# Optimization experiments

Measured on AMD Instinct MI355X. Metric: run time of the kernel, lower is better.

## Reference

```python
import jax, jax.numpy as jnp
import numpy as np

B, S, H = 2, 2048, 4096
NH, NKV, D = 32, 8, 128          # query heads, kv heads, head_dim = H // NH
G = NH // NKV                    # GQA group size
THETA = 10000.0


def setup_inputs() -> dict:
    key = jax.random.key(0)
    k1, k2, k3 = jax.random.split(key, 3)
    hidden_states = jax.random.normal(k1, (B, S, H), dtype=jnp.float32)
    positions = jnp.tile(jnp.arange(S, dtype=jnp.int64 if jax.config.jax_enable_x64 else jnp.int32), (B, 1))
    w_qkv = jax.random.normal(k2, (H, (NH + 2 * NKV) * D), dtype=jnp.float32) * 0.02
    w_o = jax.random.normal(k3, (NH * D, H), dtype=jnp.float32) * 0.02
    return {"hidden_states": hidden_states, "positions": positions, "w_qkv": w_qkv, "w_o": w_o}


def _rope_interleaved(x, positions, theta):
    # is_neox_style=False: rotate interleaved (even, odd) pairs. x: [B,S,Hh,D]
    d = x.shape[-1]
    inv_freq = 1.0 / (theta ** (jnp.arange(0, d, 2, dtype=jnp.float32) / d))  # [D/2]
    freqs = positions.astype(jnp.float32)[..., None] * inv_freq               # [B,S,D/2]
    cos = jnp.cos(freqs)[:, :, None, :]
    sin = jnp.sin(freqs)[:, :, None, :]
    x1 = x[..., 0::2]
    x2 = x[..., 1::2]
    o1 = x1 * cos - x2 * sin
    o2 = x2 * cos + x1 * sin
    return jnp.stack([o1, o2], axis=-1).reshape(x.shape)


def reference(hidden_states, positions, w_qkv, w_o):
    qkv = hidden_states @ w_qkv                                   # [B,S,(NH+2*NKV)*D]
    q, k, v = jnp.split(qkv, [NH * D, NH * D + NKV * D], axis=-1)
    q = q.reshape(B, S, NH, D)
    k = k.reshape(B, S, NKV, D)
    v = v.reshape(B, S, NKV, D)
    q = _rope_interleaved(q, positions, THETA)
    k = _rope_interleaved(k, positions, THETA)
    # GQA: group query heads per kv head instead of repeating k/v
    qg = q.reshape(B, S, NKV, G, D)
    scores = jnp.einsum('bqhgd,bkhd->bhgqk', qg, k) * (D ** -0.5)  # [B,NKV,G,S,S]
    causal = jnp.tril(jnp.ones((S, S), dtype=bool))
    scores = jnp.where(causal, scores, jnp.finfo(scores.dtype).min)
    probs = jax.nn.softmax(scores, axis=-1)
    out = jnp.einsum('bhgqk,bkhd->bqhgd', probs, v).reshape(B, S, NH * D)
    return out @ w_o                                              # [B,S,H]
```

## Files before the change

### kernel.cpp

```cpp
#include <hip/hip_runtime.h>
#include <cmath>

#define B_    2
#define S_    2048
#define H_    4096
#define NH_   32
#define NKV_  8
#define D_    128
#define QKV_N 6144
#define MTOK  4096

typedef __attribute__((ext_vector_type(8))) short bf16x8;
typedef __attribute__((ext_vector_type(4))) float f32x4;
typedef __attribute__((ext_vector_type(4))) unsigned short us4;

#define GLL16(gp, lp)                                                         \
  __builtin_amdgcn_global_load_lds(                                           \
      (const __attribute__((address_space(1))) void*)(gp),                    \
      (__attribute__((address_space(3))) void*)(lp), 16, 0, 0)

__device__ __forceinline__ unsigned short f2bf(float f) {
  unsigned u = __float_as_uint(f);
  u += 0x7fff + ((u >> 16) & 1);
  return (unsigned short)(u >> 16);
}

__global__ __launch_bounds__(256) void cast_bf16_kernel(const float* __restrict__ in,
                                                        unsigned short* __restrict__ out,
                                                        int n4) {
  int i = blockIdx.x * blockDim.x + threadIdx.x;
  if (i >= n4) return;
  float4 v = ((const float4*)in)[i];
  us4 o;
  o.x = f2bf(v.x); o.y = f2bf(v.y); o.z = f2bf(v.z); o.w = f2bf(v.w);
  ((us4*)out)[i] = o;
}

__global__ __launch_bounds__(256) void transpose_cast_kernel(const float* __restrict__ w,
                                                             unsigned short* __restrict__ wt,
                                                             int K, int N) {
  __shared__ float tile[32][33];
  const int k0 = blockIdx.y * 32, n0 = blockIdx.x * 32;
  const int tid = threadIdx.x;
  const int r = tid >> 3, c4 = (tid & 7) * 4;
  float4 v = *(const float4*)(w + (size_t)(k0 + r) * N + n0 + c4);
  tile[r][c4 + 0] = v.x; tile[r][c4 + 1] = v.y;
  tile[r][c4 + 2] = v.z; tile[r][c4 + 3] = v.w;
  __syncthreads();
  us4 o;
  o.x = f2bf(tile[c4 + 0][r]);
  o.y = f2bf(tile[c4 + 1][r]);
  o.z = f2bf(tile[c4 + 2][r]);
  o.w = f2bf(tile[c4 + 3][r]);
  *(us4*)(wt + (size_t)(n0 + r) * K + k0 + c4) = o;
}

__global__ __launch_bounds__(256) void gemm_bt_kernel(const unsigned short* __restrict__ A,
                                                      const unsigned short* __restrict__ Bt,
                                                      float* __restrict__ C,
                                                      int M, int N, int K) {
  __shared__ short As[128 * 32];
  __shared__ short Bs[128 * 32];
  const int tid = threadIdx.x;
  const int w = tid >> 6, lane = tid & 63;
  const int quad = lane >> 4, l16 = lane & 15;
  const int bm = blockIdx.y, bn = blockIdx.x;
  const int mbase = (w & 1) * 64, nbase = (w >> 1) * 64;

  f32x4 acc[4][4] = {};

  const int srow = w * 32 + (lane >> 2);
  const int skoff = (lane & 3) * 8;
  const unsigned short* Ap = A + (size_t)(bm * 128 + srow) * K + skoff;
  const unsigned short* Bp = Bt + (size_t)(bn * 128 + srow) * K + skoff;

  for (int k0 = 0; k0 < K; k0 += 32) {
    __syncthreads();
#pragma unroll
    for (int i = 0; i < 2; ++i) {
      GLL16(Ap + (size_t)i * 16 * K + k0, As + (w * 32 + i * 16) * 32);
      GLL16(Bp + (size_t)i * 16 * K + k0, Bs + (w * 32 + i * 16) * 32);
    }
    __syncthreads();
    bf16x8 af[4], bfr[4];
#pragma unroll
    for (int mi = 0; mi < 4; ++mi)
      af[mi] = *(const bf16x8*)(As + (mbase + mi * 16 + l16) * 32 + quad * 8);
#pragma unroll
    for (int nj = 0; nj < 4; ++nj)
      bfr[nj] = *(const bf16x8*)(Bs + (nbase + nj * 16 + l16) * 32 + quad * 8);
#pragma unroll
    for (int mi = 0; mi < 4; ++mi)
#pragma unroll
      for (int nj = 0; nj < 4; ++nj)
        acc[mi][nj] = __builtin_amdgcn_mfma_f32_16x16x32_bf16(af[mi], bfr[nj], acc[mi][nj], 0, 0, 0);
  }

  float* Cp = C + (size_t)(bm * 128 + mbase + quad * 4) * N + bn * 128 + nbase + l16;
#pragma unroll
  for (int mi = 0; mi < 4; ++mi)
#pragma unroll
    for (int nj = 0; nj < 4; ++nj)
#pragma unroll
      for (int r = 0; r < 4; ++r)
        Cp[(size_t)(mi * 16 + r) * N + nj * 16] = acc[mi][nj][r];
}

__global__ __launch_bounds__(256) void rope_cast_kernel(const float* __restrict__ qkv,
                                                        const int* __restrict__ positions,
                                                        unsigned short* __restrict__ qkvb) {
  const int tok = blockIdx.y;
  const int p = blockIdx.x * 256 + threadIdx.x;
  const float2 x = *(const float2*)(qkv + (size_t)tok * QKV_N + 2 * p);
  float o1, o2;
  if (p < (NH_ + NKV_) * (D_ / 2)) {
    const int j = p & 63;
    const float inv = exp2f((float)(2 * j) * (-13.287712379549449f / 128.f));
    const float f = (float)positions[tok] * inv;
    float s, c;
    sincosf(f, &s, &c);
    o1 = x.x * c - x.y * s;
    o2 = x.y * c + x.x * s;
  } else {
    o1 = x.x; o2 = x.y;
  }
  unsigned r = (unsigned)f2bf(o1) | ((unsigned)f2bf(o2) << 16);
  *(unsigned*)(qkvb + (size_t)tok * QKV_N + 2 * p) = r;
}

__global__ __launch_bounds__(256) void vtrans_kernel(const unsigned short* __restrict__ qkvb,
                                                     unsigned short* __restrict__ vT) {
  __shared__ unsigned short t[32][33];
  const int s0 = blockIdx.x * 32;
  const int y0 = blockIdx.y * 32;
  const int b = y0 >> 10;
  const int col0 = (NH_ + NKV_) * D_ + (y0 & 1023);
  const int tid = threadIdx.x;
  const int r = tid >> 3, c4 = (tid & 7) * 4;
  us4 v = *(const us4*)(qkvb + (size_t)(b * S_ + s0 + r) * QKV_N + col0 + c4);
  t[r][c4 + 0] = v.x; t[r][c4 + 1] = v.y;
  t[r][c4 + 2] = v.z; t[r][c4 + 3] = v.w;
  __syncthreads();
  us4 o;
  o.x = t[c4 + 0][r]; o.y = t[c4 + 1][r];
  o.z = t[c4 + 2][r]; o.w = t[c4 + 3][r];
  *(us4*)(vT + (size_t)(y0 + r) * S_ + s0 + c4) = o;
}

__global__ __launch_bounds__(256) void attn_mfma_kernel(const unsigned short* __restrict__ qkvb,
                                                        const unsigned short* __restrict__ vT,
                                                        unsigned short* __restrict__ aoutb) {
  __shared__ short Ks[32 * 128];
  __shared__ short Vs[128 * 32];
  const int qt = (int)gridDim.x - 1 - (int)blockIdx.x;
  const int h = blockIdx.y, b = blockIdx.z;
  const int kvh = h >> 2;
  const int tid = threadIdx.x;
  const int w = tid >> 6, lane = tid & 63;
  const int quad = lane >> 4, l16 = lane & 15;

  const int qrow = qt * 64 + w * 16 + l16;
  const unsigned short* qp = qkvb + (size_t)(b * S_ + qrow) * QKV_N + h * D_ + quad * 8;
  bf16x8 qf[4];
#pragma unroll
  for (int kk = 0; kk < 4; ++kk) qf[kk] = *(const bf16x8*)(qp + kk * 32);

  unsigned ks0, ks1, vs0, vs1;
  {
    int i0 = w * 64 + lane;
    int i1 = i0 + 256;
    int r0 = i0 >> 4, c0 = i0 & 15;
    int r1 = i1 >> 4, c1 = i1 & 15;
    int cs0 = (c0 & 8) | ((c0 ^ r0) & 7);
    int cs1 = (c1 & 8) | ((c1 ^ r1) & 7);
    ks0 = (unsigned)(b * S_ + r0) * QKV_N + NH_ * D_ + kvh * D_ + cs0 * 8;
    ks1 = (unsigned)(b * S_ + r1) * QKV_N + NH_ * D_ + kvh * D_ + cs1 * 8;
    int vr0 = i0 >> 2, vc0 = i0 & 3;
    int vr1 = i1 >> 2, vc1 = i1 & 3;
    int vcs0 = vc0 ^ ((vr0 & 3) ^ ((vr0 >> 2) & 3));
    int vcs1 = vc1 ^ ((vr1 & 3) ^ ((vr1 >> 2) & 3));
    vs0 = (unsigned)((b * NKV_ + kvh) * D_ + vr0) * S_ + vcs0 * 8;
    vs1 = (unsigned)((b * NKV_ + kvh) * D_ + vr1) * S_ + vcs1 * 8;
  }
  short* KsW = Ks + w * 512;
  short* VsW = Vs + w * 512;

  const int kbase = l16 * 128 + ((quad ^ (l16 & 3)) << 3);
  const int mh5 = ((l16 >> 2) & 1) << 5;
  const int swl = (l16 & 3) ^ ((l16 >> 2) & 3);
  const int vbase = l16 * 32 + ((quad ^ swl) << 3);

  float m = -1e30f, lsum = 0.f;
  f32x4 oacc[8] = {};

  const int qminw = qt * 64 + w * 16;
  const int qmaxw = qminw + 15;
  const int ntiles = 2 * qt + 2;
  const float SCL = 0.08838834764831845f * 1.4426950408889634f;

  for (int kt = 0; kt < ntiles; ++kt) {
    const int kb = kt * 32;
    __syncthreads();
    {
      const unsigned short* kgp = qkvb + (size_t)kb * QKV_N;
      GLL16(kgp + ks0, KsW);
      GLL16(kgp + ks1, KsW + 2048);
      GLL16(vT + vs0 + kb, VsW);
      GLL16(vT + vs1 + kb, VsW + 2048);
    }
    __syncthreads();
    if (kb <= qmaxw) {
      f32x4 st0 = {}, st1 = {};
#pragma unroll
      for (int kk = 0; kk < 4; ++kk) {
        const int ko = (kk << 5) ^ mh5;
        bf16x8 kf0 = *(const bf16x8*)(Ks + kbase + ko);
        bf16x8 kf1 = *(const bf16x8*)(Ks + kbase + 2048 + ko);
        st0 = __builtin_amdgcn_mfma_f32_16x16x32_bf16(kf0, qf[kk], st0, 0, 0, 0);
        st1 = __builtin_amdgcn_mfma_f32_16x16x32_bf16(kf1, qf[kk], st1, 0, 0, 0);
      }
      float sc[8];
#pragma unroll
      for (int r = 0; r < 4; ++r) {
        sc[r] = st0[r] * SCL;
        sc[4 + r] = st1[r] * SCL;
      }
      if (kb + 31 > qminw) {
        const int kvb0 = kb + quad * 4;
#pragma unroll
        for (int r = 0; r < 4; ++r) {
          if (kvb0 + r > qrow) sc[r] = -1e30f;
          if (kvb0 + 16 + r > qrow) sc[4 + r] = -1e30f;
        }
      }
      float cmax = sc[0];
#pragma unroll
      for (int i = 1; i < 8; ++i) cmax = fmaxf(cmax, sc[i]);
      cmax = fmaxf(cmax, __shfl_xor(cmax, 16));
      cmax = fmaxf(cmax, __shfl_xor(cmax, 32));
      const float mn = fmaxf(m, cmax);
      const float alpha = exp2f(m - mn);
      m = mn;
      float p[8];
      float ps = 0.f;
#pragma unroll
      for (int i = 0; i < 8; ++i) { p[i] = exp2f(sc[i] - mn); ps += p[i]; }
      lsum = lsum * alpha + ps;
      unsigned pw00 = (unsigned)f2bf(p[0]) | ((unsigned)f2bf(p[1]) << 16);
      unsigned pw01 = (unsigned)f2bf(p[2]) | ((unsigned)f2bf(p[3]) << 16);
      unsigned pw10 = (unsigned)f2bf(p[4]) | ((unsigned)f2bf(p[5]) << 16);
      unsigned pw11 = (unsigned)f2bf(p[6]) | ((unsigned)f2bf(p[7]) << 16);
      const int srcA = l16 + ((quad & 1) << 5);
      const int srcB = srcA + 16;
      unsigned g0 = __shfl(pw00, srcA), g1 = __shfl(pw01, srcA);
      unsigned g2 = __shfl(pw10, srcA), g3 = __shfl(pw11, srcA);
      unsigned h0 = __shfl(pw00, srcB), h1 = __shfl(pw01, srcB);
      unsigned h2 = __shfl(pw10, srcB), h3 = __shfl(pw11, srcB);
      const bool loq = quad < 2;
      union { unsigned u[4]; bf16x8 v; } pu;
      pu.u[0] = loq ? g0 : g2;
      pu.u[1] = loq ? g1 : g3;
      pu.u[2] = loq ? h0 : h2;
      pu.u[3] = loq ? h1 : h3;
      const bf16x8 pf = pu.v;
      const int abase = (lane & 48) | (quad << 2);
      const float al0 = __shfl(alpha, abase);
      const float al1 = __shfl(alpha, abase + 1);
      const float al2 = __shfl(alpha, abase + 2);
      const float al3 = __shfl(alpha, abase + 3);
#pragma unroll
      for (int n2 = 0; n2 < 8; ++n2) {
        oacc[n2][0] *= al0; oacc[n2][1] *= al1;
        oacc[n2][2] *= al2; oacc[n2][3] *= al3;
        bf16x8 vf = *(const bf16x8*)(Vs + vbase + n2 * 512);
        oacc[n2] = __builtin_amdgcn_mfma_f32_16x16x32_bf16(pf, vf, oacc[n2], 0, 0, 0);
      }
    }
  }
  lsum += __shfl_xor(lsum, 16);
  lsum += __shfl_xor(lsum, 32);
  const float inv = 1.f / lsum;
  const int abase = (lane & 48) | (quad << 2);
  const float i0 = __shfl(inv, abase), i1 = __shfl(inv, abase + 1);
  const float i2 = __shfl(inv, abase + 2), i3 = __shfl(inv, abase + 3);
  unsigned short* op = aoutb + (size_t)(b * S_ + qt * 64 + w * 16 + quad * 4) * (NH_ * D_) + h * D_ + l16;
#pragma unroll
  for (int n2 = 0; n2 < 8; ++n2) {
    op[0 * (NH_ * D_) + n2 * 16] = f2bf(oacc[n2][0] * i0);
    op[1 * (NH_ * D_) + n2 * 16] = f2bf(oacc[n2][1] * i1);
    op[2 * (NH_ * D_) + n2 * 16] = f2bf(oacc[n2][2] * i2);
    op[3 * (NH_ * D_) + n2 * 16] = f2bf(oacc[n2][3] * i3);
  }
}

extern "C" void kernel_launch(void* const* d_in, const int* in_sizes, int n_in,
                              void* d_out, int out_size, void* d_ws, size_t ws_size,
                              hipStream_t stream) {
  const float* hs    = (const float*)d_in[0];
  const int*   pos   = (const int*)d_in[1];
  const float* w_qkv = (const float*)d_in[2];
  const float* w_o   = (const float*)d_in[3];
  float* out = (float*)d_out;

  char* wsp = (char*)d_ws;
  float* qkv           = (float*)wsp;
  unsigned short* qkvb = (unsigned short*)(wsp + (size_t)MTOK * QKV_N * 4);
  unsigned short* bufB = (unsigned short*)(wsp + (size_t)MTOK * QKV_N * 6);
  unsigned short* bufC = bufB + (size_t)MTOK * H_;
  unsigned short* vT   = bufC + (size_t)MTOK * QKV_N;

  cast_bf16_kernel<<<(MTOK * H_ / 4 + 255) / 256, 256, 0, stream>>>(hs, bufB, MTOK * H_ / 4);
  {
    dim3 g(QKV_N / 32, H_ / 32);
    transpose_cast_kernel<<<g, 256, 0, stream>>>(w_qkv, bufC, H_, QKV_N);
  }

  {
    dim3 g(QKV_N / 128, MTOK / 128);
    gemm_bt_kernel<<<g, 256, 0, stream>>>(bufB, bufC, qkv, MTOK, QKV_N, H_);
  }

  {
    dim3 g((QKV_N / 2) / 256, MTOK);
    rope_cast_kernel<<<g, 256, 0, stream>>>(qkv, pos, qkvb);
  }

  {
    dim3 g(S_ / 32, (B_ * NKV_ * D_) / 32);
    vtrans_kernel<<<g, 256, 0, stream>>>(qkvb, vT);
  }

  {
    dim3 ga(S_ / 64, NH_, B_);
    attn_mfma_kernel<<<ga, 256, 0, stream>>>(qkvb, vT, bufC);
  }

  {
    dim3 g(H_ / 32, H_ / 32);
    transpose_cast_kernel<<<g, 256, 0, stream>>>(w_o, bufB, H_, H_);
  }

  {
    dim3 g(H_ / 128, MTOK / 128);
    gemm_bt_kernel<<<g, 256, 0, stream>>>(bufC, bufB, out, MTOK, H_, NH_ * D_);
  }
}
```

Baseline: 1.096 ms.

## Double-buffer attention KV tiles, enlarge query tile, and XCD-aware block remap

Attention now processes 128 query rows per block (32 per wave, two MFMA row groups), which halves the number of times each K/V tile is loaded relative to the query work done on it. K/V tiles are double-buffered in LDS, with the next tile prefetched before computing the current one using explicit vmcnt waits and raw barriers. Wave priority is raised around MFMA sections. Both the GEMM and the attention launch remap block indices so that neighbouring tiles land on the same XCD for L2 reuse. This costs more registers and LDS and can lower occupancy. The causal work per block is also coarser, so load imbalance grows.

```diff
diff --git a/kernel.cpp b/kernel.cpp
--- a/kernel.cpp
+++ b/kernel.cpp
@@ -64,7 +64,12 @@
   const int tid = threadIdx.x;
   const int w = tid >> 6, lane = tid & 63;
   const int quad = lane >> 4, l16 = lane & 15;
-  const int bm = blockIdx.y, bn = blockIdx.x;
+  const int nx = (int)gridDim.x;
+  const int nwg = nx * (int)gridDim.y;
+  const int oid = (int)blockIdx.y * nx + (int)blockIdx.x;
+  const int cpx = nwg >> 3;
+  const int sid = (oid & 7) * cpx + (oid >> 3);
+  const int bn = sid % nx, bm = sid / nx;
   const int mbase = (w & 1) * 64, nbase = (w >> 1) * 64;
 
   f32x4 acc[4][4] = {};
@@ -150,20 +155,29 @@
 __global__ __launch_bounds__(256) void attn_mfma_kernel(const unsigned short* __restrict__ qkvb,
                                                         const unsigned short* __restrict__ vT,
                                                         unsigned short* __restrict__ aoutb) {
-  __shared__ short Ks[32 * 128];
-  __shared__ short Vs[128 * 32];
-  const int qt = (int)gridDim.x - 1 - (int)blockIdx.x;
-  const int h = blockIdx.y, b = blockIdx.z;
+  __shared__ short Ks[2][32 * 128];
+  __shared__ short Vs[2][32 * 128];
+  const int p = (int)blockIdx.x;
+  const int o = ((p >> 3) & 63) + 64 * ((p & 7) + 8 * (p >> 9));
+  const int qt = 15 - (o & 15);
+  const int h = (o >> 4) & 31;
+  const int b = o >> 9;
   const int kvh = h >> 2;
   const int tid = threadIdx.x;
   const int w = tid >> 6, lane = tid & 63;
   const int quad = lane >> 4, l16 = lane & 15;
-
-  const int qrow = qt * 64 + w * 16 + l16;
-  const unsigned short* qp = qkvb + (size_t)(b * S_ + qrow) * QKV_N + h * D_ + quad * 8;
-  bf16x8 qf[4];
-#pragma unroll
-  for (int kk = 0; kk < 4; ++kk) qf[kk] = *(const bf16x8*)(qp + kk * 32);
+  const int qbase = qt * 128 + w * 32;
+
+  bf16x8 qf0[4], qf1[4];
+  {
+    const unsigned short* qp0 = qkvb + (size_t)(b * S_ + qbase + l16) * QKV_N + h * D_ + quad * 8;
+    const unsigned short* qp1 = qp0 + (size_t)16 * QKV_N;
+#pragma unroll
+    for (int kk = 0; kk < 4; ++kk) {
+      qf0[kk] = *(const bf16x8*)(qp0 + kk * 32);
+      qf1[kk] = *(const bf16x8*)(qp1 + kk * 32);
+    }
+  }
 
   unsigned ks0, ks1, vs0, vs1;
   {
@@ -182,115 +196,157 @@
     vs0 = (unsigned)((b * NKV_ + kvh) * D_ + vr0) * S_ + vcs0 * 8;
     vs1 = (unsigned)((b * NKV_ + kvh) * D_ + vr1) * S_ + vcs1 * 8;
   }
-  short* KsW = Ks + w * 512;
-  short* VsW = Vs + w * 512;
+
+#define STAGE_KV(bufi, kbv)                                                   \
+  {                                                                           \
+    const unsigned short* kgp_ = qkvb + (size_t)(kbv) * QKV_N;                \
+    short* KsW_ = &Ks[bufi][w * 512];                                         \
+    short* VsW_ = &Vs[bufi][w * 512];                                         \
+    GLL16(kgp_ + ks0, KsW_);                                                  \
+    GLL16(kgp_ + ks1, KsW_ + 2048);                                           \
+    GLL16(vT + vs0 + (kbv), VsW_);                                            \
+    GLL16(vT + vs1 + (kbv), VsW_ + 2048);                                     \
+  }
 
   const int kbase = l16 * 128 + ((quad ^ (l16 & 3)) << 3);
   const int mh5 = ((l16 >> 2) & 1) << 5;
   const int swl = (l16 & 3) ^ ((l16 >> 2) & 3);
   const int vbase = l16 * 32 + ((quad ^ swl) << 3);
 
-  float m = -1e30f, lsum = 0.f;
-  f32x4 oacc[8] = {};
-
-  const int qminw = qt * 64 + w * 16;
-  const int qmaxw = qminw + 15;
-  const int ntiles = 2 * qt + 2;
+  float mreg[2] = {-1e30f, -1e30f};
+  float lreg[2] = {0.f, 0.f};
+  f32x4 oacc0[8] = {};
+  f32x4 oacc1[8] = {};
+
+  const int qmaxw = qbase + 31;
+  const int ntiles = 4 * qt + 4;
   const float SCL = 0.08838834764831845f * 1.4426950408889634f;
 
+  STAGE_KV(0, 0);
   for (int kt = 0; kt < ntiles; ++kt) {
     const int kb = kt * 32;
-    __syncthreads();
-    {
-      const unsigned short* kgp = qkvb + (size_t)kb * QKV_N;
-      GLL16(kgp + ks0, KsW);
-      GLL16(kgp + ks1, KsW + 2048);
-      GLL16(vT + vs0 + kb, VsW);
-      GLL16(vT + vs1 + kb, VsW + 2048);
+    const int cur = kt & 1;
+    if (kt + 1 < ntiles) {
+      STAGE_KV(cur ^ 1, kb + 32);
+      asm volatile("s_waitcnt vmcnt(4)" ::: "memory");
+    } else {
+      asm volatile("s_waitcnt vmcnt(0)" ::: "memory");
     }
-    __syncthreads();
+    __builtin_amdgcn_s_barrier();
     if (kb <= qmaxw) {
-      f32x4 st0 = {}, st1 = {};
+      const short* Kc = Ks[cur];
+      const short* Vc = Vs[cur];
+      f32x4 st00 = {}, st01 = {}, st10 = {}, st11 = {};
+      __builtin_amdgcn_s_setprio(1);
 #pragma unroll
       for (int kk = 0; kk < 4; ++kk) {
         const int ko = (kk << 5) ^ mh5;
-        bf16x8 kf0 = *(const bf16x8*)(Ks + kbase + ko);
-        bf16x8 kf1 = *(const bf16x8*)(Ks + kbase + 2048 + ko);
-        st0 = __builtin_amdgcn_mfma_f32_16x16x32_bf16(kf0, qf[kk], st0, 0, 0, 0);
-        st1 = __builtin_amdgcn_mfma_f32_16x16x32_bf16(kf1, qf[kk], st1, 0, 0, 0);
+        bf16x8 kf0 = *(const bf16x8*)(Kc + kbase + ko);
+        bf16x8 kf1 = *(const bf16x8*)(Kc + kbase + 2048 + ko);
+        st00 = __builtin_amdgcn_mfma_f32_16x16x32_bf16(kf0, qf0[kk], st00, 0, 0, 0);
+        st01 = __builtin_amdgcn_mfma_f32_16x16x32_bf16(kf1, qf0[kk], st01, 0, 0, 0);
+        st10 = __builtin_amdgcn_mfma_f32_16x16x32_bf16(kf0, qf1[kk], st10, 0, 0, 0);
+        st11 = __builtin_amdgcn_mfma_f32_16x16x32_bf16(kf1, qf1[kk], st11, 0, 0, 0);
       }
-      float sc[8];
-#pragma unroll
-      for (int r = 0; r < 4; ++r) {
-        sc[r] = st0[r] * SCL;
-        sc[4 + r] = st1[r] * SCL;
+      __builtin_amdgcn_s_setprio(0);
+      bf16x8 pf[2];
+      float al[2][4];
+#pragma unroll
+      for (int s = 0; s < 2; ++s) {
+        const f32x4 a0 = s ? st10 : st00;
+        const f32x4 a1 = s ? st11 : st01;
+        float sc[8];
+#pragma unroll
+        for (int r = 0; r < 4; ++r) {
+          sc[r] = a0[r] * SCL;
+          sc[4 + r] = a1[r] * SCL;
+        }
+        const int qrow = qbase + s * 16 + l16;
+        if (kb + 31 > qbase + s * 16) {
+          const int kvb0 = kb + quad * 4;
+#pragma unroll
+          for (int r = 0; r < 4; ++r) {
+            if (kvb0 + r > qrow) sc[r] = -1e30f;
+            if (kvb0 + 16 + r > qrow) sc[4 + r] = -1e30f;
+          }
+        }
+        float cmax = sc[0];
+#pragma unroll
+        for (int i = 1; i < 8; ++i) cmax = fmaxf(cmax, sc[i]);
+        cmax = fmaxf(cmax, __shfl_xor(cmax, 16));
+        cmax = fmaxf(cmax, __shfl_xor(cmax, 32));
+        const float mo = mreg[s];
+        const float mn = fmaxf(mo, cmax);
+        const float alpha = exp2f(mo - mn);
+        mreg[s] = mn;
+        float pr[8];
+        float ps = 0.f;
+#pragma unroll
+        for (int i = 0; i < 8; ++i) { pr[i] = exp2f(sc[i] - mn); ps += pr[i]; }
+        lreg[s] = lreg[s] * alpha + ps;
+        unsigned pw00 = (unsigned)f2bf(pr[0]) | ((unsigned)f2bf(pr[1]) << 16);
+        unsigned pw01 = (unsigned)f2bf(pr[2]) | ((unsigned)f2bf(pr[3]) << 16);
+        unsigned pw10 = (unsigned)f2bf(pr[4]) | ((unsigned)f2bf(pr[5]) << 16);
+        unsigned pw11 = (unsigned)f2bf(pr[6]) | ((unsigned)f2bf(pr[7]) << 16);
+        const int srcA = l16 + ((quad & 1) << 5);
+        const int srcB = srcA + 16;
+        unsigned g0 = __shfl(pw00, srcA), g1 = __shfl(pw01, srcA);
+        unsigned g2 = __shfl(pw10, srcA), g3 = __shfl(pw11, srcA);
+        unsigned h0 = __shfl(pw00, srcB), h1 = __shfl(pw01, srcB);
+        unsigned h2 = __shfl(pw10, srcB), h3 = __shfl(pw11, srcB);
+        const bool loq = quad < 2;
+        union { unsigned u[4]; bf16x8 v; } pu;
+        pu.u[0] = loq ? g0 : g2;
+        pu.u[1] = loq ? g1 : g3;
+        pu.u[2] = loq ? h0 : h2;
+        pu.u[3] = loq ? h1 : h3;
+        pf[s] = pu.v;
+        const int abase = (lane & 48) | (quad << 2);
+        al[s][0] = __shfl(alpha, abase);
+        al[s][1] = __shfl(alpha, abase + 1);
+        al[s][2] = __shfl(alpha, abase + 2);
+        al[s][3] = __shfl(alpha, abase + 3);
       }
-      if (kb + 31 > qminw) {
-        const int kvb0 = kb + quad * 4;
-#pragma unroll
-        for (int r = 0; r < 4; ++r) {
-          if (kvb0 + r > qrow) sc[r] = -1e30f;
-          if (kvb0 + 16 + r > qrow) sc[4 + r] = -1e30f;
-        }
+      __builtin_amdgcn_s_setprio(1);
+#pragma unroll
+      for (int n2 = 0; n2 < 8; ++n2) {
+        bf16x8 vf = *(const bf16x8*)(Vc + vbase + n2 * 512);
+        oacc0[n2][0] *= al[0][0]; oacc0[n2][1] *= al[0][1];
+        oacc0[n2][2] *= al[0][2]; oacc0[n2][3] *= al[0][3];
+        oacc0[n2] = __builtin_amdgcn_mfma_f32_16x16x32_bf16(pf[0], vf, oacc0[n2], 0, 0, 0);
+        oacc1[n2][0] *= al[1][0]; oacc1[n2][1] *= al[1][1];
+        oacc1[n2][2] *= al[1][2]; oacc1[n2][3] *= al[1][3];
+        oacc1[n2] = __builtin_amdgcn_mfma_f32_16x16x32_bf16(pf[1], vf, oacc1[n2], 0, 0, 0);
       }
-      float cmax = sc[0];
-#pragma unroll
-      for (int i = 1; i < 8; ++i) cmax = fmaxf(cmax, sc[i]);
-      cmax = fmaxf(cmax, __shfl_xor(cmax, 16));
-      cmax = fmaxf(cmax, __shfl_xor(cmax, 32));
-      const float mn = fmaxf(m, cmax);
-      const float alpha = exp2f(m - mn);
-      m = mn;
-      float p[8];
-      float ps = 0.f;
-#pragma unroll
-      for (int i = 0; i < 8; ++i) { p[i] = exp2f(sc[i] - mn); ps += p[i]; }
-      lsum = lsum * alpha + ps;
-      unsigned pw00 = (unsigned)f2bf(p[0]) | ((unsigned)f2bf(p[1]) << 16);
-      unsigned pw01 = (unsigned)f2bf(p[2]) | ((unsigned)f2bf(p[3]) << 16);
-      unsigned pw10 = (unsigned)f2bf(p[4]) | ((unsigned)f2bf(p[5]) << 16);
-      unsigned pw11 = (unsigned)f2bf(p[6]) | ((unsigned)f2bf(p[7]) << 16);
-      const int srcA = l16 + ((quad & 1) << 5);
-      const int srcB = srcA + 16;
-      unsigned g0 = __shfl(pw00, srcA), g1 = __shfl(pw01, srcA);
-      unsigned g2 = __shfl(pw10, srcA), g3 = __shfl(pw11, srcA);
-      unsigned h0 = __shfl(pw00, srcB), h1 = __shfl(pw01, srcB);
-      unsigned h2 = __shfl(pw10, srcB), h3 = __shfl(pw11, srcB);
-      const bool loq = quad < 2;
-      union { unsigned u[4]; bf16x8 v; } pu;
-      pu.u[0] = loq ? g0 : g2;
-      pu.u[1] = loq ? g1 : g3;
-      pu.u[2] = loq ? h0 : h2;
-      pu.u[3] = loq ? h1 : h3;
-      const bf16x8 pf = pu.v;
-      const int abase = (lane & 48) | (quad << 2);
-      const float al0 = __shfl(alpha, abase);
-      const float al1 = __shfl(alpha, abase + 1);
-      const float al2 = __shfl(alpha, abase + 2);
-      const float al3 = __shfl(alpha, abase + 3);
-#pragma unroll
-      for (int n2 = 0; n2 < 8; ++n2) {
-        oacc[n2][0] *= al0; oacc[n2][1] *= al1;
-        oacc[n2][2] *= al2; oacc[n2][3] *= al3;
-        bf16x8 vf = *(const bf16x8*)(Vs + vbase + n2 * 512);
-        oacc[n2] = __builtin_amdgcn_mfma_f32_16x16x32_bf16(pf, vf, oacc[n2], 0, 0, 0);
-      }
+      __builtin_amdgcn_s_setprio(0);
     }
-  }
-  lsum += __shfl_xor(lsum, 16);
-  lsum += __shfl_xor(lsum, 32);
-  const float inv = 1.f / lsum;
-  const int abase = (lane & 48) | (quad << 2);
-  const float i0 = __shfl(inv, abase), i1 = __shfl(inv, abase + 1);
-  const float i2 = __shfl(inv, abase + 2), i3 = __shfl(inv, abase + 3);
-  unsigned short* op = aoutb + (size_t)(b * S_ + qt * 64 + w * 16 + quad * 4) * (NH_ * D_) + h * D_ + l16;
-#pragma unroll
-  for (int n2 = 0; n2 < 8; ++n2) {
-    op[0 * (NH_ * D_) + n2 * 16] = f2bf(oacc[n2][0] * i0);
-    op[1 * (NH_ * D_) + n2 * 16] = f2bf(oacc[n2][1] * i1);
-    op[2 * (NH_ * D_) + n2 * 16] = f2bf(oacc[n2][2] * i2);
-    op[3 * (NH_ * D_) + n2 * 16] = f2bf(oacc[n2][3] * i3);
-  }
+    __builtin_amdgcn_s_barrier();
+  }
+
+#define ATTN_EPI(sI, OA)                                                      \
+  {                                                                           \
+    float lsv = lreg[sI];                                                     \
+    lsv += __shfl_xor(lsv, 16);                                               \
+    lsv += __shfl_xor(lsv, 32);                                               \
+    const float inv = 1.f / lsv;                                              \
+    const int ab_ = (lane & 48) | (quad << 2);                                \
+    const float i0 = __shfl(inv, ab_), i1 = __shfl(inv, ab_ + 1);             \
+    const float i2 = __shfl(inv, ab_ + 2), i3 = __shfl(inv, ab_ + 3);         \
+    unsigned short* op = aoutb +                                              \
+        (size_t)(b * S_ + qbase + sI * 16 + quad * 4) * (NH_ * D_) +          \
+        h * D_ + l16;                                                         \
+    _Pragma("unroll")                                                         \
+    for (int n2 = 0; n2 < 8; ++n2) {                                          \
+      op[0 * (NH_ * D_) + n2 * 16] = f2bf(OA[n2][0] * i0);                    \
+      op[1 * (NH_ * D_) + n2 * 16] = f2bf(OA[n2][1] * i1);                    \
+      op[2 * (NH_ * D_) + n2 * 16] = f2bf(OA[n2][2] * i2);                    \
+      op[3 * (NH_ * D_) + n2 * 16] = f2bf(OA[n2][3] * i3);                    \
+    }                                                                         \
+  }
+  ATTN_EPI(0, oacc0);
+  ATTN_EPI(1, oacc1);
+#undef ATTN_EPI
+#undef STAGE_KV
 }
 
 extern "C" void kernel_launch(void* const* d_in, const int* in_sizes, int n_in,
@@ -331,7 +387,7 @@
   }
 
   {
-    dim3 ga(S_ / 64, NH_, B_);
+    dim3 ga((S_ / 128) * NH_ * B_);
     attn_mfma_kernel<<<ga, 256, 0, stream>>>(qkvb, vT, bufC);
   }
 
```

Measured after the change: 1.092 ms. No clear change (-0.4%).
